# Kernel optimization log

Hardware: AMD Instinct MI355X
Metric: run time of the kernel (lower is better)

## Reference

```python
import jax, jax.numpy as jnp
import numpy as np

GAMMA = 2
EPS = 1e-8


def setup_inputs() -> dict:
    key = jax.random.key(0)
    kx, kw = jax.random.split(key)
    B, C, D, W, H = 4, 256, 16, 16, 16
    x = jax.random.normal(kx, (B, C, D, W, H), dtype=jnp.float32)
    # Conv3d(chan, chan, kernel_size=1) == per-voxel linear: weight (C_out, C_in), bias (C_out,)
    Wt = jax.random.normal(kw, (C, C), dtype=jnp.float32) * 0.02
    b = jnp.zeros((C,), dtype=jnp.float32)
    return {"x": x, "W": Wt, "b": b}


def reference(x, W, b):
    B, C, D, Wd, H = x.shape
    N = D * Wd * H
    xf = x.reshape(B, C, N)                                  # b c n
    # torch cosine_similarity(dim=1): dot / max(|xi|*|xj|, eps)
    norm = jnp.linalg.norm(xf, axis=1, keepdims=True)        # b 1 n
    xn = xf / jnp.maximum(norm, EPS)
    sim = jnp.einsum('bcn,bcm->bnm', xn, xn)                 # b n n (cosine)
    sim = jax.nn.relu(sim) ** GAMMA
    # transform_net: 1x1x1 conv = channel-mixing GEMM per voxel
    t = jnp.einsum('oc,bcm->bom', W, xf) + b[None, :, None]  # b c m
    out = jnp.einsum('bnm,bcm->bcn', sim, t)                 # b c n
    return out.reshape(B, C, D, Wd, H)
```

## Files before the change

### kernel.cpp

```cpp
#include <hip/hip_runtime.h>
#include <hip/hip_bf16.h>


typedef unsigned short u16;
typedef __attribute__((ext_vector_type(8))) short short8;
typedef __attribute__((ext_vector_type(4))) float f32x4;

#define MFMA16(a, b, c) __builtin_amdgcn_mfma_f32_16x16x32_bf16((a), (b), (c), 0, 0, 0)

__device__ __forceinline__ u16 f2bf(float f) {
    union { float f; unsigned u; } v; v.f = f;
    unsigned u = v.u;
    u += 0x7fffu + ((u >> 16) & 1u);
    return (u16)(u >> 16);
}

__device__ __forceinline__ unsigned cvtpk(float lo, float hi) {
    unsigned r;
    asm("v_cvt_pk_bf16_f32 %0, %1, %2" : "=v"(r) : "v"(lo), "v"(hi));
    return r;
}

__global__ __launch_bounds__(256) void k_prep(const float* __restrict__ x,
                                              const float* __restrict__ W,
                                              u16* __restrict__ xff,
                                              u16* __restrict__ Wf,
                                              float* __restrict__ nrm) {
    __shared__ float xs[256][65];
    __shared__ float part[4][64];
    __shared__ float rs_s[64];
    int bid = blockIdx.x;
    int b = bid >> 6, nt = bid & 63, n0 = nt << 6;
    int tid = threadIdx.x;

    if (bid < 32) {
        int q = (bid << 8) + tid;
        int lane = q & 63, kc = (q >> 6) & 7, ci = (q >> 9) & 3, wq = q >> 11;
        int row = (wq << 6) + (ci << 4) + (lane & 15);
        int col = (kc << 5) + ((lane >> 4) << 3);
        const float* wp = W + row * 256 + col;
        u16 tmp[8];
#pragma unroll
        for (int j = 0; j < 8; ++j) tmp[j] = f2bf(wp[j]);
        *(short8*)(Wf + ((size_t)q << 3)) = *(const short8*)tmp;
    }

    int rowg = tid >> 4, l16 = tid & 15;
    const float* xb = x + ((size_t)b << 20) + n0;
#pragma unroll
    for (int s = 0; s < 16; ++s) {
        int row = (s << 4) + rowg;
        float4 v = *(const float4*)(xb + (size_t)row * 4096 + (l16 << 2));
        xs[row][(l16 << 2) + 0] = v.x;
        xs[row][(l16 << 2) + 1] = v.y;
        xs[row][(l16 << 2) + 2] = v.z;
        xs[row][(l16 << 2) + 3] = v.w;
    }
    __syncthreads();
    int q2 = tid >> 6, nl = tid & 63;
    float ss = 0.f;
#pragma unroll 16
    for (int c = 0; c < 64; ++c) {
        float v = xs[(q2 << 6) + c][nl];
        ss += v * v;
    }
    part[q2][nl] = ss;
    __syncthreads();
    if (tid < 64) {
        float t = part[0][tid] + part[1][tid] + part[2][tid] + part[3][tid];
        float nr = sqrtf(t);
        nrm[(b << 12) + n0 + tid] = nr;
        rs_s[tid] = 1.0f / fmaxf(nr, 1e-8f);
    }
    __syncthreads();

    u16* xo = xff + ((size_t)b << 20) + ((size_t)nt << 14);
    int lane = tid & 63;
#pragma unroll
    for (int s = 0; s < 8; ++s) {
        int w2 = (s << 2) + (tid >> 6);
        int tl = ((w2 & 3) << 4) + (tid & 15);
        int c8 = ((w2 >> 2) << 2) + ((tid >> 4) & 3);
        float rsv = rs_s[tl];
        u16 tmp[8];
#pragma unroll
        for (int j = 0; j < 8; ++j)
            tmp[j] = f2bf(xs[(c8 << 3) + j][tl] * rsv);
        int chunk = ((tl >> 4) << 3) + (c8 >> 2);
        *(short8*)(xo + (chunk << 9) + (lane << 3)) = *(const short8*)tmp;
    }
}

__global__ __launch_bounds__(256) void k_tgemm(const u16* __restrict__ Wf,
                                               const u16* __restrict__ xff,
                                               const float* __restrict__ bias,
                                               const float* __restrict__ nrm,
                                               u16* __restrict__ tbf) {
    __shared__ u16 lds_t[256][72];
    int bid = blockIdx.x;
    int b = bid >> 6, mt = bid & 63;
    const u16* xf_t = xff + ((size_t)b << 20) + ((size_t)mt << 14);
    int tid = threadIdx.x, wid = tid >> 6, lane = tid & 63, lg = lane >> 4, lr = lane & 15;

    f32x4 zero = {0.f, 0.f, 0.f, 0.f};
    f32x4 acc[4][4];
#pragma unroll
    for (int ci = 0; ci < 4; ++ci)
#pragma unroll
        for (int mj = 0; mj < 4; ++mj) acc[ci][mj] = zero;

#pragma unroll
    for (int kc = 0; kc < 8; ++kc) {
        short8 afr[4], bfr[4];
#pragma unroll
        for (int ci = 0; ci < 4; ++ci)
            afr[ci] = *(const short8*)(Wf + ((size_t)((((wid << 2) + ci) << 3) + kc) << 9)
                                       + (lane << 3));
#pragma unroll
        for (int mj = 0; mj < 4; ++mj)
            bfr[mj] = *(const short8*)(xf_t + ((size_t)(((mj << 3) + kc)) << 9)
                                       + (lane << 3));
#pragma unroll
        for (int ci = 0; ci < 4; ++ci)
#pragma unroll
            for (int mj = 0; mj < 4; ++mj)
                acc[ci][mj] = MFMA16(afr[ci], bfr[mj], acc[ci][mj]);
    }
    float nv[4];
#pragma unroll
    for (int mj = 0; mj < 4; ++mj)
        nv[mj] = nrm[(b << 12) + (mt << 6) + (mj << 4) + lr];
#pragma unroll
    for (int ci = 0; ci < 4; ++ci) {
#pragma unroll
        for (int r = 0; r < 4; ++r) {
            int c = (wid << 6) + (ci << 4) + (lg << 2) + r;
            float bv = bias[c];
#pragma unroll
            for (int mj = 0; mj < 4; ++mj)
                lds_t[c][(mj << 4) + lr] = f2bf(acc[ci][mj][r] * nv[mj] + bv);
        }
    }
    __syncthreads();
    u16* to = tbf + ((size_t)b << 20) + ((size_t)mt << 14);
#pragma unroll
    for (int s = 0; s < 8; ++s) {
        int w2 = (s << 2) + (tid >> 6);
        int cq = w2 >> 3, ci2 = (w2 >> 1) & 3, k2 = w2 & 1;
        short8 v = *(const short8*)(&lds_t[(cq << 6) + (ci2 << 4) + lr][(k2 << 5) + (lg << 3)]);
        *(short8*)(to + (w2 << 9) + (lane << 3)) = v;
    }
}

__global__ __launch_bounds__(512) void k_fused(const u16* __restrict__ xff,
                                               const u16* __restrict__ tbf,
                                               float* __restrict__ out) {
    __shared__ __align__(16) u16 lds_p[4][4096];

#define PBYTE(row, col) ((((row) << 7) + ((col) << 1)) ^ (((row) & 7) << 4))
#define BAR() do { asm volatile("s_waitcnt lgkmcnt(0)" ::: "memory");              \
    __builtin_amdgcn_sched_barrier(0); __builtin_amdgcn_s_barrier();               \
    __builtin_amdgcn_sched_barrier(0); } while (0)

    int bid = blockIdx.x;
    int xcd = bid & 7, grp = bid >> 3;
    int batch = xcd >> 1;
    int nt = grp + 32 * (xcd & 1);
    int n0 = nt << 6;

    const u16* xf_b = xff + ((size_t)batch << 20);
    const u16* tb_f = tbf + ((size_t)batch << 20);
    float* out_b = out + ((size_t)batch << 20);

    int tid = threadIdx.x;
    int wid = tid >> 6, lane = tid & 63, lg = lane >> 4, lr = lane & 15;
    int lane8 = lane << 3;
    f32x4 zero = {0.f, 0.f, 0.f, 0.f};
    char* pbase = (char*)&lds_p[0][0];

    if (wid < 4) {
        int tc = wid;
        int colw = (tc << 4) + lr;
        short8 afrag[4][8];
#pragma unroll
        for (int rt = 0; rt < 4; ++rt)
#pragma unroll
            for (int kc = 0; kc < 8; ++kc)
                afrag[rt][kc] = *(const short8*)(xf_b
                    + ((size_t)((((nt << 2) + rt) << 3) + kc) << 9) + lane8);
        const u16* bb = xf_b + ((size_t)(tc << 3) << 9);
        short8 bfrA[8], bfrB[8];

#define RLDB(BUF, OFF)                                                                     \
        { _Pragma("unroll")                                                                \
          for (int kc = 0; kc < 8; ++kc)                                                   \
              BUF[kc] = *(const short8*)(bb + (OFF) + (kc << 9) + lane8); }

#define SCOMP(BUF, SLOT)                                                                   \
    {                                                                                      \
        f32x4 sac[4];                                                                      \
        _Pragma("unroll") for (int c = 0; c < 4; ++c) sac[c] = zero;                       \
        __builtin_amdgcn_s_setprio(1);                                                     \
        _Pragma("unroll")                                                                  \
        for (int kc = 0; kc < 8; ++kc) {                                                   \
            sac[0] = MFMA16(afrag[0][kc], BUF[kc], sac[0]);                                \
            sac[1] = MFMA16(afrag[1][kc], BUF[kc], sac[1]);                                \
            sac[2] = MFMA16(afrag[2][kc], BUF[kc], sac[2]);                                \
            sac[3] = MFMA16(afrag[3][kc], BUF[kc], sac[3]);                                \
        }                                                                                  \
        __builtin_amdgcn_s_setprio(0);                                                     \
        char* pd = pbase + ((SLOT) << 13);                                                 \
        _Pragma("unroll")                                                                  \
        for (int c = 0; c < 4; ++c) {                                                      \
            float q0 = fmaxf(sac[c][0], 0.f); q0 *= q0;                                    \
            float q1 = fmaxf(sac[c][1], 0.f); q1 *= q1;                                    \
            float q2 = fmaxf(sac[c][2], 0.f); q2 *= q2;                                    \
            float q3 = fmaxf(sac[c][3], 0.f); q3 *= q3;                                    \
            unsigned d01 = cvtpk(q0, q1);                                                  \
            unsigned d23 = cvtpk(q2, q3);                                                  \
            int rw = (lg << 2) + (c << 4);                                                 \
            *(u16*)(pd + PBYTE(rw, colw)) = (u16)d01;                                      \
            *(u16*)(pd + PBYTE(rw + 1, colw)) = (u16)(d01 >> 16);                          \
            *(u16*)(pd + PBYTE(rw + 2, colw)) = (u16)d23;                                  \
            *(u16*)(pd + PBYTE(rw + 3, colw)) = (u16)(d23 >> 16);                          \
        }                                                                                  \
    }

        RLDB(bfrA, 0);
        RLDB(bfrB, 16384);
        bb += 32768;
        SCOMP(bfrA, 0);
        RLDB(bfrA, 0);
        SCOMP(bfrB, 1);
        RLDB(bfrB, 16384);
        bb += 32768;
        BAR();

        for (int pp = 0; pp < 15; ++pp) {
            SCOMP(bfrA, 2);
            RLDB(bfrA, 0);
            SCOMP(bfrB, 3);
            RLDB(bfrB, 16384);
            bb += 32768;
            BAR();
            SCOMP(bfrA, 0);
            RLDB(bfrA, 0);
            SCOMP(bfrB, 1);
            RLDB(bfrB, 16384);
            bb += 32768;
            BAR();
        }
        SCOMP(bfrA, 2);
        SCOMP(bfrB, 3);
        BAR();
        BAR();
#undef SCOMP
#undef RLDB
    } else {
        int cq = wid - 4;
        const u16* tbse = tb_f + ((size_t)(cq << 3) << 9);
        short8 tbcA[4][2], tbcB[4][2];

#define RLDT(TB, OFF)                                                                      \
        { _Pragma("unroll")                                                                \
          for (int ci = 0; ci < 4; ++ci) {                                                 \
              _Pragma("unroll")                                                            \
              for (int k2 = 0; k2 < 2; ++k2)                                               \
                  TB[ci][k2] = *(const short8*)(tbse + (OFF)                               \
                                                + ((((ci << 1) + k2)) << 9) + lane8); } }

#define RDP(PFR, SLOT)                                                                     \
    {                                                                                      \
        char* pc = pbase + ((SLOT) << 13);                                                 \
        _Pragma("unroll")                                                                  \
        for (int nj = 0; nj < 4; ++nj) {                                                   \
            PFR[nj][0] = *(const short8*)(pc + PBYTE((nj << 4) + lr, (lg << 3)));          \
            PFR[nj][1] = *(const short8*)(pc + PBYTE((nj << 4) + lr, 32 + (lg << 3)));     \
        }                                                                                  \
    }

#define OMMA(TC, PFR)                                                                      \
    {                                                                                      \
        __builtin_amdgcn_s_setprio(1);                                                     \
        _Pragma("unroll")                                                                  \
        for (int ci = 0; ci < 4; ++ci) {                                                   \
            _Pragma("unroll")                                                              \
            for (int nj = 0; nj < 4; ++nj) {                                               \
                oacc[ci][nj] = MFMA16(TC[ci][0], PFR[nj][0], oacc[ci][nj]);                \
                oacc[ci][nj] = MFMA16(TC[ci][1], PFR[nj][1], oacc[ci][nj]);                \
            }                                                                              \
        }                                                                                  \
        __builtin_amdgcn_s_setprio(0);                                                     \
    }

        RLDT(tbcA, 0);
        RLDT(tbcB, 16384);
        tbse += 32768;

        f32x4 oacc[4][4];
#pragma unroll
        for (int ci = 0; ci < 4; ++ci)
#pragma unroll
            for (int nj = 0; nj < 4; ++nj) oacc[ci][nj] = zero;
        BAR();

        for (int pp = 0; pp < 15; ++pp) {
            {
                short8 pfrA[4][2], pfrB[4][2];
                RDP(pfrA, 0);
                RDP(pfrB, 1);
                OMMA(tbcA, pfrA);
                RLDT(tbcA, 0);
                OMMA(tbcB, pfrB);
                RLDT(tbcB, 16384);
                tbse += 32768;
                BAR();
            }
            {
                short8 pfrA[4][2], pfrB[4][2];
                RDP(pfrA, 2);
                RDP(pfrB, 3);
                OMMA(tbcA, pfrA);
                RLDT(tbcA, 0);
                OMMA(tbcB, pfrB);
                RLDT(tbcB, 16384);
                tbse += 32768;
                BAR();
            }
        }
        {
            short8 pfrA[4][2], pfrB[4][2];
            RDP(pfrA, 0);
            RDP(pfrB, 1);
            OMMA(tbcA, pfrA);
            RLDT(tbcA, 0);
            OMMA(tbcB, pfrB);
            RLDT(tbcB, 16384);
            BAR();
        }
        {
            short8 pfrA[4][2], pfrB[4][2];
            RDP(pfrA, 2);
            RDP(pfrB, 3);
            OMMA(tbcA, pfrA);
            OMMA(tbcB, pfrB);
            BAR();
        }
#undef OMMA
#undef RDP
#undef RLDT

#pragma unroll
        for (int ci = 0; ci < 4; ++ci) {
            int c = (cq << 6) + (ci << 4) + (lg << 2);
#pragma unroll
            for (int nj = 0; nj < 4; ++nj) {
                int n = n0 + (nj << 4) + lr;
                float* op = out_b + (size_t)c * 4096 + n;
#pragma unroll
                for (int r = 0; r < 4; ++r) op[(size_t)r * 4096] = oacc[ci][nj][r];
            }
        }
    }
#undef PBYTE
#undef BAR
}

extern "C" void kernel_launch(void* const* d_in, const int* in_sizes, int n_in,
                              void* d_out, int out_size, void* d_ws, size_t ws_size,
                              hipStream_t stream) {
    const float* x = (const float*)d_in[0];
    const float* W = (const float*)d_in[1];
    const float* bias = (const float*)d_in[2];
    float* out = (float*)d_out;

    char* ws = (char*)d_ws;
    u16* xff = (u16*)ws;
    u16* tbf = (u16*)(ws + ((size_t)8 << 20));
    u16* Wf = (u16*)(ws + ((size_t)16 << 20));
    float* nrm = (float*)(ws + ((size_t)16 << 20) + (192u << 10));

    hipLaunchKernelGGL(k_prep, dim3(256), dim3(256), 0, stream, x, W, xff, Wf, nrm);
    hipLaunchKernelGGL(k_tgemm, dim3(256), dim3(256), 0, stream, Wf, xff, bias, nrm, tbf);
    hipLaunchKernelGGL(k_fused, dim3(256), dim3(512), 0, stream, xff, tbf, out);
}
```

Measured before the change: 77.11 us.

## Fuse prep and transform GEMM kernels; double P-tile LDS slots per barrier

Merges the normalization/prep kernel with the transform GEMM so the bf16 x fragments and norms stay in shared memory, and converts W to bf16 on the fly instead of through a separate buffer. This removes one launch and the global round trip of xff, nrm and Wf. Separately, the fused kernel's P buffer grows from 4 to 8 slots, so each barrier phase now processes four sub-tiles instead of two, halving the number of barriers. The costs are much higher LDS use in the prep kernel (lower occupancy), redundant W conversion in every block, and more LDS in the fused kernel.

```diff
diff --git a/kernel.cpp b/kernel.cpp
--- a/kernel.cpp
+++ b/kernel.cpp
@@ -21,29 +21,22 @@
     return r;
 }
 
-__global__ __launch_bounds__(256) void k_prep(const float* __restrict__ x,
-                                              const float* __restrict__ W,
-                                              u16* __restrict__ xff,
-                                              u16* __restrict__ Wf,
-                                              float* __restrict__ nrm) {
+__global__ __launch_bounds__(256) void k_prep2(const float* __restrict__ x,
+                                               const float* __restrict__ W,
+                                               const float* __restrict__ bias,
+                                               u16* __restrict__ xff,
+                                               u16* __restrict__ tbf) {
     __shared__ float xs[256][65];
     __shared__ float part[4][64];
     __shared__ float rs_s[64];
+    __shared__ float nrm_s[64];
+    __shared__ __align__(16) u16 xfrag[32][512];
+    __shared__ u16 lds_t[256][72];
+
     int bid = blockIdx.x;
     int b = bid >> 6, nt = bid & 63, n0 = nt << 6;
     int tid = threadIdx.x;
-
-    if (bid < 32) {
-        int q = (bid << 8) + tid;
-        int lane = q & 63, kc = (q >> 6) & 7, ci = (q >> 9) & 3, wq = q >> 11;
-        int row = (wq << 6) + (ci << 4) + (lane & 15);
-        int col = (kc << 5) + ((lane >> 4) << 3);
-        const float* wp = W + row * 256 + col;
-        u16 tmp[8];
-#pragma unroll
-        for (int j = 0; j < 8; ++j) tmp[j] = f2bf(wp[j]);
-        *(short8*)(Wf + ((size_t)q << 3)) = *(const short8*)tmp;
-    }
+    int wid = tid >> 6, lane = tid & 63, lg = lane >> 4, lr = lane & 15;
 
     int rowg = tid >> 4, l16 = tid & 15;
     const float* xb = x + ((size_t)b << 20) + n0;
@@ -69,13 +62,12 @@
     if (tid < 64) {
         float t = part[0][tid] + part[1][tid] + part[2][tid] + part[3][tid];
         float nr = sqrtf(t);
-        nrm[(b << 12) + n0 + tid] = nr;
+        nrm_s[tid] = nr;
         rs_s[tid] = 1.0f / fmaxf(nr, 1e-8f);
     }
     __syncthreads();
 
     u16* xo = xff + ((size_t)b << 20) + ((size_t)nt << 14);
-    int lane = tid & 63;
 #pragma unroll
     for (int s = 0; s < 8; ++s) {
         int w2 = (s << 2) + (tid >> 6);
@@ -88,19 +80,9 @@
             tmp[j] = f2bf(xs[(c8 << 3) + j][tl] * rsv);
         int chunk = ((tl >> 4) << 3) + (c8 >> 2);
         *(short8*)(xo + (chunk << 9) + (lane << 3)) = *(const short8*)tmp;
-    }
-}
-
-__global__ __launch_bounds__(256) void k_tgemm(const u16* __restrict__ Wf,
-                                               const u16* __restrict__ xff,
-                                               const float* __restrict__ bias,
-                                               const float* __restrict__ nrm,
-                                               u16* __restrict__ tbf) {
-    __shared__ u16 lds_t[256][72];
-    int bid = blockIdx.x;
-    int b = bid >> 6, mt = bid & 63;
-    const u16* xf_t = xff + ((size_t)b << 20) + ((size_t)mt << 14);
-    int tid = threadIdx.x, wid = tid >> 6, lane = tid & 63, lg = lane >> 4, lr = lane & 15;
+        *(short8*)(&xfrag[chunk][lane << 3]) = *(const short8*)tmp;
+    }
+    __syncthreads();
 
     f32x4 zero = {0.f, 0.f, 0.f, 0.f};
     f32x4 acc[4][4];
@@ -113,13 +95,20 @@
     for (int kc = 0; kc < 8; ++kc) {
         short8 afr[4], bfr[4];
 #pragma unroll
-        for (int ci = 0; ci < 4; ++ci)
-            afr[ci] = *(const short8*)(Wf + ((size_t)((((wid << 2) + ci) << 3) + kc) << 9)
-                                       + (lane << 3));
+        for (int ci = 0; ci < 4; ++ci) {
+            const float* wp = W + (((wid << 6) + (ci << 4) + lr) << 8) + (kc << 5) + (lg << 3);
+            float4 w0 = *(const float4*)wp;
+            float4 w1 = *(const float4*)(wp + 4);
+            union { unsigned u[4]; short8 s; } uw;
+            uw.u[0] = cvtpk(w0.x, w0.y);
+            uw.u[1] = cvtpk(w0.z, w0.w);
+            uw.u[2] = cvtpk(w1.x, w1.y);
+            uw.u[3] = cvtpk(w1.z, w1.w);
+            afr[ci] = uw.s;
+        }
 #pragma unroll
         for (int mj = 0; mj < 4; ++mj)
-            bfr[mj] = *(const short8*)(xf_t + ((size_t)(((mj << 3) + kc)) << 9)
-                                       + (lane << 3));
+            bfr[mj] = *(const short8*)(&xfrag[(mj << 3) + kc][lane << 3]);
 #pragma unroll
         for (int ci = 0; ci < 4; ++ci)
 #pragma unroll
@@ -129,7 +118,7 @@
     float nv[4];
 #pragma unroll
     for (int mj = 0; mj < 4; ++mj)
-        nv[mj] = nrm[(b << 12) + (mt << 6) + (mj << 4) + lr];
+        nv[mj] = nrm_s[(mj << 4) + lr];
 #pragma unroll
     for (int ci = 0; ci < 4; ++ci) {
 #pragma unroll
@@ -142,7 +131,7 @@
         }
     }
     __syncthreads();
-    u16* to = tbf + ((size_t)b << 20) + ((size_t)mt << 14);
+    u16* to = tbf + ((size_t)b << 20) + ((size_t)nt << 14);
 #pragma unroll
     for (int s = 0; s < 8; ++s) {
         int w2 = (s << 2) + (tid >> 6);
@@ -155,7 +144,7 @@
 __global__ __launch_bounds__(512) void k_fused(const u16* __restrict__ xff,
                                                const u16* __restrict__ tbf,
                                                float* __restrict__ out) {
-    __shared__ __align__(16) u16 lds_p[4][4096];
+    __shared__ __align__(16) u16 lds_p[8][4096];
 
 #define PBYTE(row, col) ((((row) << 7) + ((col) << 1)) ^ (((row) & 7) << 4))
 #define BAR() do { asm volatile("s_waitcnt lgkmcnt(0)" ::: "memory");              \
@@ -226,34 +215,27 @@
         }                                                                                  \
     }
 
+#define PPH_FULL(S0, S1, S2, S3)                                                           \
+        SCOMP(bfrA, S0); RLDB(bfrA, 2 * 16384);                                            \
+        SCOMP(bfrB, S1); RLDB(bfrB, 3 * 16384);                                            \
+        SCOMP(bfrA, S2); RLDB(bfrA, 4 * 16384);                                            \
+        SCOMP(bfrB, S3); RLDB(bfrB, 5 * 16384);                                            \
+        bb += 4 * 16384; BAR();
+
         RLDB(bfrA, 0);
         RLDB(bfrB, 16384);
-        bb += 32768;
-        SCOMP(bfrA, 0);
-        RLDB(bfrA, 0);
-        SCOMP(bfrB, 1);
-        RLDB(bfrB, 16384);
-        bb += 32768;
-        BAR();
-
-        for (int pp = 0; pp < 15; ++pp) {
-            SCOMP(bfrA, 2);
-            RLDB(bfrA, 0);
-            SCOMP(bfrB, 3);
-            RLDB(bfrB, 16384);
-            bb += 32768;
-            BAR();
-            SCOMP(bfrA, 0);
-            RLDB(bfrA, 0);
-            SCOMP(bfrB, 1);
-            RLDB(bfrB, 16384);
-            bb += 32768;
-            BAR();
-        }
-        SCOMP(bfrA, 2);
-        SCOMP(bfrB, 3);
+        PPH_FULL(0, 1, 2, 3);
+        for (int pp = 0; pp < 7; ++pp) {
+            PPH_FULL(4, 5, 6, 7);
+            PPH_FULL(0, 1, 2, 3);
+        }
+        SCOMP(bfrA, 4); RLDB(bfrA, 2 * 16384);
+        SCOMP(bfrB, 5); RLDB(bfrB, 3 * 16384);
+        SCOMP(bfrA, 6);
+        SCOMP(bfrB, 7);
         BAR();
         BAR();
+#undef PPH_FULL
 #undef SCOMP
 #undef RLDB
     } else {
@@ -293,10 +275,26 @@
         __builtin_amdgcn_s_setprio(0);                                                     \
     }
 
+#define CPH(S0, S1, S2, S3, MODE)                                                          \
+    {                                                                                      \
+        short8 pfA[4][2], pfB[4][2];                                                       \
+        RDP(pfA, S0); RDP(pfB, S1);                                                        \
+        OMMA(tbcA, pfA);                                                                   \
+        if ((MODE) >= 1) RLDT(tbcA, 2 * 16384);                                            \
+        RDP(pfA, S2);                                                                      \
+        OMMA(tbcB, pfB);                                                                   \
+        if ((MODE) >= 1) RLDT(tbcB, 3 * 16384);                                            \
+        RDP(pfB, S3);                                                                      \
+        OMMA(tbcA, pfA);                                                                   \
+        if ((MODE) >= 2) RLDT(tbcA, 4 * 16384);                                            \
+        OMMA(tbcB, pfB);                                                                   \
+        if ((MODE) >= 2) RLDT(tbcB, 5 * 16384);                                            \
+        if ((MODE) >= 2) tbse += 4 * 16384;                                                \
+        BAR();                                                                             \
+    }
+
         RLDT(tbcA, 0);
         RLDT(tbcB, 16384);
-        tbse += 32768;
-
         f32x4 oacc[4][4];
 #pragma unroll
         for (int ci = 0; ci < 4; ++ci)
@@ -304,48 +302,13 @@
             for (int nj = 0; nj < 4; ++nj) oacc[ci][nj] = zero;
         BAR();
 
-        for (int pp = 0; pp < 15; ++pp) {
-            {
-                short8 pfrA[4][2], pfrB[4][2];
-                RDP(pfrA, 0);
-                RDP(pfrB, 1);
-                OMMA(tbcA, pfrA);
-                RLDT(tbcA, 0);
-                OMMA(tbcB, pfrB);
-                RLDT(tbcB, 16384);
-                tbse += 32768;
-                BAR();
-            }
-            {
-                short8 pfrA[4][2], pfrB[4][2];
-                RDP(pfrA, 2);
-                RDP(pfrB, 3);
-                OMMA(tbcA, pfrA);
-                RLDT(tbcA, 0);
-                OMMA(tbcB, pfrB);
-                RLDT(tbcB, 16384);
-                tbse += 32768;
-                BAR();
-            }
-        }
-        {
-            short8 pfrA[4][2], pfrB[4][2];
-            RDP(pfrA, 0);
-            RDP(pfrB, 1);
-            OMMA(tbcA, pfrA);
-            RLDT(tbcA, 0);
-            OMMA(tbcB, pfrB);
-            RLDT(tbcB, 16384);
-            BAR();
-        }
-        {
-            short8 pfrA[4][2], pfrB[4][2];
-            RDP(pfrA, 2);
-            RDP(pfrB, 3);
-            OMMA(tbcA, pfrA);
-            OMMA(tbcB, pfrB);
-            BAR();
-        }
+        for (int pp = 0; pp < 7; ++pp) {
+            CPH(0, 1, 2, 3, 2);
+            CPH(4, 5, 6, 7, 2);
+        }
+        CPH(0, 1, 2, 3, 2);
+        CPH(4, 5, 6, 7, 1);
+#undef CPH
 #undef OMMA
 #undef RDP
 #undef RLDT
@@ -377,10 +340,7 @@
     char* ws = (char*)d_ws;
     u16* xff = (u16*)ws;
     u16* tbf = (u16*)(ws + ((size_t)8 << 20));
-    u16* Wf = (u16*)(ws + ((size_t)16 << 20));
-    float* nrm = (float*)(ws + ((size_t)16 << 20) + (192u << 10));
-
-    hipLaunchKernelGGL(k_prep, dim3(256), dim3(256), 0, stream, x, W, xff, Wf, nrm);
-    hipLaunchKernelGGL(k_tgemm, dim3(256), dim3(256), 0, stream, Wf, xff, bias, nrm, tbf);
+
+    hipLaunchKernelGGL(k_prep2, dim3(256), dim3(256), 0, stream, x, W, bias, xff, tbf);
     hipLaunchKernelGGL(k_fused, dim3(256), dim3(512), 0, stream, xff, tbf, out);
 }
```

Result: slower. 81.86 us (+6.2%).
